# Kernel tuning notes

Measured on AMD Instinct MI355X. Metric: run time of the kernel, lower is better.

The kernel has to match this reference:

```python
import jax, jax.numpy as jnp
import numpy as np

N_CELLS = 50000
HID = 64
DEG = 16
K_NODES = 4  # nodes per cell; cell i owns nodes [4i, 4i+4)
SP = 3


def setup_inputs() -> dict:
    key = jax.random.key(0)
    ks = jax.random.split(key, 12)
    s = 1.0 / np.sqrt(HID)
    inp = {
        'features': jax.random.normal(ks[0], (N_CELLS, HID), jnp.float32),
        'positions': jax.random.normal(ks[1], (K_NODES * N_CELLS, SP), jnp.float32),
        'neighbors': jax.random.randint(ks[2], (N_CELLS, DEG), 0, N_CELLS, jnp.int32),
        # message MLP: Linear(2H+1 -> H), SiLU, Linear(H -> H)
        'W1': jax.random.normal(ks[3], (2 * HID + 1, HID), jnp.float32) * s,
        'b1': jnp.zeros((HID,), jnp.float32),
        'W2': jax.random.normal(ks[4], (HID, HID), jnp.float32) * s,
        'b2': jnp.zeros((HID,), jnp.float32),
        # update MLP: Linear(H + H -> H), SiLU, Linear(H -> H)
        'Wu1': jax.random.normal(ks[5], (2 * HID, HID), jnp.float32) * s,
        'bu1': jnp.zeros((HID,), jnp.float32),
        'Wu2': jax.random.normal(ks[6], (HID, HID), jnp.float32) * s,
        'bu2': jnp.zeros((HID,), jnp.float32),
    }
    return inp


def reference(features, positions, neighbors, W1, b1, W2, b2, Wu1, bu1, Wu2, bu2):
    N, H = features.shape
    # centroid of each cell's owned nodes (cell i -> nodes [K*i, K*i+K))
    cent = positions.reshape(N, K_NODES, SP).mean(axis=1)          # [N, sp]
    fj = features[neighbors]                                       # [N, D, H]
    cj = cent[neighbors]                                           # [N, D, sp]
    # centroid-distance geometric invariant per (cell, neighbor) pair
    geom = jnp.linalg.norm(cent[:, None, :] - cj, axis=-1, keepdims=True)  # [N, D, 1]
    fi = jnp.broadcast_to(features[:, None, :], fj.shape)          # [N, D, H]
    x = jnp.concatenate([fi, fj, geom], axis=-1)                   # [N, D, 2H+1]
    h = jax.nn.silu(x @ W1 + b1) @ W2 + b2                         # [N, D, H]
    msg = h.mean(axis=1)                                           # mean over neighbors
    u = jnp.concatenate([features, msg], axis=-1)                  # [N, 2H]
    upd = jax.nn.silu(u @ Wu1 + bu1) @ Wu2 + bu2
    updated_features = features + upd
    return updated_features, positions
```

## Files before the change

### kernel.cpp

```cpp
#include <hip/hip_runtime.h>


#define DEG 16

typedef __attribute__((ext_vector_type(8))) short short8;
typedef __attribute__((ext_vector_type(4))) float f32x4;
typedef uint2 uint2_a __attribute__((may_alias));
typedef uint4 uint4_a __attribute__((may_alias));

union HbRd { uint4_a u; short8 s; };
union Frag { short8 s; uint4 u; };

__device__ __forceinline__ unsigned f2bf(float f) {
  unsigned u = __float_as_uint(f);
  return (u + 0x7FFFu + ((u >> 16) & 1u)) >> 16;
}
__device__ __forceinline__ float bf2f(unsigned bits16) {
  return __uint_as_float(bits16 << 16);
}
__device__ __forceinline__ float silu(float h) {
  return h / (1.f + __expf(-h));
}
__device__ __forceinline__ float silu_fast(float h) {
  return h * __builtin_amdgcn_rcpf(1.f + __expf(-h));
}

__global__ __launch_bounds__(256) void aux_kernel(
    const float* __restrict__ pos,
    const float* __restrict__ W1, const float* __restrict__ W2,
    const float* __restrict__ Wu1, const float* __restrict__ Wu2,
    float* __restrict__ outpos, float* __restrict__ cent4,
    unsigned short* __restrict__ w1pq, unsigned short* __restrict__ w2t,
    unsigned short* __restrict__ wu1t, unsigned short* __restrict__ wu2b)
{
  int t = blockIdx.x * 256 + threadIdx.x;
  if (t < 150000) {
    ((float4*)outpos)[t] = ((const float4*)pos)[t];
  } else if (t < 174576) {
    const int r = t - 150000;
    if (r < 8192) {
      const int j = r & 7, l = (r >> 3) & 15, q = (r >> 7) & 3;
      const int f = r >> 9, kk = f & 1, mt = f >> 1;
      const int k = kk * 32 + q * 8 + j;
      const int m = mt * 16 + l;
      w1pq[r] = (unsigned short)f2bf(
          (m < 64) ? W1[k * 64 + m] : W1[(k + 64) * 64 + (m - 64)]);
    } else if (r < 12288) {
      const int s = r - 8192;
      const int j = s & 7, l = (s >> 3) & 15, q = (s >> 7) & 3;
      const int f = s >> 9, kk = f & 1, mt = f >> 1;
      const int k = kk * 32 + q * 8 + j;
      w2t[s] = (unsigned short)f2bf(W2[k * 64 + mt * 16 + l]);
    } else if (r < 20480) {
      const int s = r - 12288;
      const int j = s & 7, l = (s >> 3) & 15, q = (s >> 7) & 3;
      const int f = s >> 9, kk = f & 3, mt = f >> 2;
      const int k = kk * 32 + q * 8 + j;
      wu1t[s] = (unsigned short)f2bf(Wu1[k * 64 + mt * 16 + l]);
    } else {
      const int s = r - 20480;
      const int j = s & 7, l = (s >> 3) & 15, q = (s >> 7) & 3;
      const int f = s >> 9, kk = f & 1, nt = f >> 1;
      const int k = kk * 32 + q * 8 + j;
      wu2b[s] = (unsigned short)f2bf(Wu2[k * 64 + nt * 16 + l]);
    }
  } else if (t < 224576) {
    const int i = t - 174576;
    const float4* pp = (const float4*)(pos + 12 * i);
    const float4 a = pp[0], b = pp[1], c = pp[2];
    float4 o;
    o.x = (a.x + a.w + b.z + c.y) * 0.25f;
    o.y = (a.y + b.x + b.w + c.z) * 0.25f;
    o.z = (a.z + b.y + c.x + c.w) * 0.25f;
    o.w = 0.f;
    ((float4*)cent4)[i] = o;
  }
}

__global__ __launch_bounds__(256) void prep_geom_kernel(
    const float* __restrict__ feat,
    const unsigned short* __restrict__ w1pq,
    const float4* __restrict__ cent4,
    const int* __restrict__ nbr,
    unsigned short* __restrict__ featb,
    unsigned short* __restrict__ Pb, unsigned char* __restrict__ Q8,
    float* __restrict__ geomF)
{
  const int b    = blockIdx.x;
  const int lane = threadIdx.x & 63;
  const int wid  = threadIdx.x >> 6;

  if (b >= 782) {
    const int gb  = b - 782;
    const int sub = lane >> 4;
    const int d   = lane & 15;
    const int c   = gb * 16 + wid * 4 + sub;
    const int nj  = nbr[c * DEG + d];
    const float4 ci = cent4[c];
    const float4 cj = cent4[nj];
    const float dx = ci.x - cj.x, dy = ci.y - cj.y, dz = ci.z - cj.z;
    geomF[c * DEG + d] = sqrtf(dx * dx + dy * dy + dz * dz);
    return;
  }

  const int quad = lane >> 4;
  const int l15  = lane & 15;
  const int tile = b * 4 + wid;
  const bool act = (tile < 3125);
  const int  tt  = act ? tile : 3124;
  const int  cr  = tt * 16 + l15;

  short8 xf[2];
  #pragma unroll
  for (int kk = 0; kk < 2; ++kk) {
    const float4 f0 = *(const float4*)(feat + cr * 64 + kk * 32 + quad * 8);
    const float4 f1 = *(const float4*)(feat + cr * 64 + kk * 32 + quad * 8 + 4);
    Frag v;
    v.s[0] = (short)f2bf(f0.x); v.s[1] = (short)f2bf(f0.y);
    v.s[2] = (short)f2bf(f0.z); v.s[3] = (short)f2bf(f0.w);
    v.s[4] = (short)f2bf(f1.x); v.s[5] = (short)f2bf(f1.y);
    v.s[6] = (short)f2bf(f1.z); v.s[7] = (short)f2bf(f1.w);
    xf[kk] = v.s;
    if (act) *(uint4*)(featb + cr * 64 + kk * 32 + quad * 8) = v.u;
  }

  short8 wf[8][2];
  #pragma unroll
  for (int mt = 0; mt < 8; ++mt)
    #pragma unroll
    for (int kk = 0; kk < 2; ++kk)
      wf[mt][kk] = *(const short8*)(w1pq + (((mt * 2 + kk) * 4 + quad) << 7) + l15 * 8);

  f32x4 acc[8] = {};
  #pragma unroll
  for (int kk = 0; kk < 2; ++kk)
    #pragma unroll
    for (int mt = 0; mt < 8; ++mt)
      acc[mt] = __builtin_amdgcn_mfma_f32_16x16x32_bf16(wf[mt][kk], xf[kk], acc[mt], 0, 0, 0);

  if (act) {
    #pragma unroll
    for (int mt = 0; mt < 4; ++mt) {
      uint2 pk;
      pk.x = f2bf(acc[mt][0]) | (f2bf(acc[mt][1]) << 16);
      pk.y = f2bf(acc[mt][2]) | (f2bf(acc[mt][3]) << 16);
      *(uint2*)(Pb + cr * 64 + mt * 16 + quad * 4) = pk;
    }
    #pragma unroll
    for (int mt = 4; mt < 8; ++mt) {
      int w = __builtin_amdgcn_cvt_pk_fp8_f32(acc[mt][0], acc[mt][1], 0, false);
      w = __builtin_amdgcn_cvt_pk_fp8_f32(acc[mt][2], acc[mt][3], w, true);
      *(unsigned int*)(Q8 + cr * 64 + (mt - 4) * 16 + quad * 4) = (unsigned)w;
    }
  }
}

__global__ __launch_bounds__(256) void gather_kernel(
    const unsigned short* __restrict__ Pb,
    const unsigned char* __restrict__ Q8,
    const float* __restrict__ geomF,
    const int* __restrict__ nbr,
    const float* __restrict__ b1, const float* __restrict__ W1,
    unsigned short* __restrict__ sB)
{
  const int lane = threadIdx.x & 63;
  const int wid  = threadIdx.x >> 6;
  const int c    = blockIdx.x * 4 + wid;

  const int   nj = nbr[c * DEG + (lane & 15)];
  const float gv = geomF[c * DEG + (lane & 15)];

  const float pcb = bf2f(Pb[c * 64 + lane]) + b1[lane];
  const float wl  = W1[8192 + lane];

  float acc = 0.f;
  #pragma unroll
  for (int d = 0; d < DEG; ++d) {
    const int   nd = __builtin_amdgcn_readlane(nj, d);
    const float gd = __uint_as_float(
        __builtin_amdgcn_readlane((int)__float_as_uint(gv), d));
    const float qv = __builtin_amdgcn_cvt_f32_fp8((int)Q8[nd * 64 + lane], 0);
    acc += silu_fast(pcb + qv + gd * wl);
  }

  sB[c * 64 + lane] = (unsigned short)f2bf(acc * 0.0625f);
}

__global__ __launch_bounds__(256) void tail_kernel(
    const unsigned short* __restrict__ featb,
    const unsigned short* __restrict__ sB,
    const float* __restrict__ feat,
    const unsigned short* __restrict__ w2t,
    const unsigned short* __restrict__ wu1t,
    const unsigned short* __restrict__ wu2b,
    const float* __restrict__ b2, const float* __restrict__ bu1,
    const float* __restrict__ bu2,
    float* __restrict__ outf)
{
  __shared__ uint4 smem[4 * 288];
  const int lane = threadIdx.x & 63;
  const int wid  = threadIdx.x >> 6;
  const int quad = lane >> 4;
  const int l15  = lane & 15;
  char* Msg = (char*)(smem + wid * 288);
  char* Hb  = Msg + 2304;

  short8 w2f[4][2];
  #pragma unroll
  for (int mt = 0; mt < 4; ++mt)
    #pragma unroll
    for (int kk = 0; kk < 2; ++kk)
      w2f[mt][kk] = *(const short8*)(w2t + (((mt * 2 + kk) * 4 + quad) << 7) + l15 * 8);
  short8 wu1f[4][4];
  #pragma unroll
  for (int mt = 0; mt < 4; ++mt)
    #pragma unroll
    for (int kk = 0; kk < 4; ++kk)
      wu1f[mt][kk] = *(const short8*)(wu1t + (((mt * 4 + kk) * 4 + quad) << 7) + l15 * 8);
  short8 wu2f[4][2];
  #pragma unroll
  for (int nt = 0; nt < 4; ++nt)
    #pragma unroll
    for (int kk = 0; kk < 2; ++kk)
      wu2f[nt][kk] = *(const short8*)(wu2b + (((nt * 2 + kk) * 4 + quad) << 7) + l15 * 8);

  f32x4 b2f[4], bu1f[4];
  #pragma unroll
  for (int mt = 0; mt < 4; ++mt) {
    b2f[mt]  = *(const f32x4*)(b2  + mt * 16 + quad * 4);
    bu1f[mt] = *(const f32x4*)(bu1 + mt * 16 + quad * 4);
  }
  float bu2v[4];
  #pragma unroll
  for (int nt = 0; nt < 4; ++nt) bu2v[nt] = bu2[nt * 16 + l15];

  const int tile = blockIdx.x * 4 + wid;
  const bool act = (tile < 3125);
  const int  tt  = act ? tile : 3124;
  const int  cr  = tt * 16 + l15;

  f32x4 accm[4] = {};
  #pragma unroll
  for (int kk = 0; kk < 2; ++kk) {
    const short8 bf = *(const short8*)(sB + cr * 64 + kk * 32 + quad * 8);
    #pragma unroll
    for (int mt = 0; mt < 4; ++mt)
      accm[mt] = __builtin_amdgcn_mfma_f32_16x16x32_bf16(w2f[mt][kk], bf, accm[mt], 0, 0, 0);
  }
  #pragma unroll
  for (int mt = 0; mt < 4; ++mt) {
    uint2 pk;
    pk.x = f2bf(accm[mt][0] + b2f[mt][0]) | (f2bf(accm[mt][1] + b2f[mt][1]) << 16);
    pk.y = f2bf(accm[mt][2] + b2f[mt][2]) | (f2bf(accm[mt][3] + b2f[mt][3]) << 16);
    *(uint2_a*)(Msg + l15 * 144 + mt * 32 + quad * 8) = pk;
  }
  __threadfence_block();

  f32x4 accu[4] = {};
  #pragma unroll
  for (int kk = 0; kk < 4; ++kk) {
    short8 bf;
    if (kk < 2) {
      bf = *(const short8*)(featb + cr * 64 + kk * 32 + quad * 8);
    } else {
      HbRd t; t.u = *(const uint4_a*)(Msg + l15 * 144 + (kk - 2) * 64 + quad * 16);
      bf = t.s;
    }
    #pragma unroll
    for (int mt = 0; mt < 4; ++mt)
      accu[mt] = __builtin_amdgcn_mfma_f32_16x16x32_bf16(wu1f[mt][kk], bf, accu[mt], 0, 0, 0);
  }
  #pragma unroll
  for (int mt = 0; mt < 4; ++mt) {
    float sv[4];
    #pragma unroll
    for (int rg = 0; rg < 4; ++rg)
      sv[rg] = silu(accu[mt][rg] + bu1f[mt][rg]);
    uint2 pk;
    pk.x = f2bf(sv[0]) | (f2bf(sv[1]) << 16);
    pk.y = f2bf(sv[2]) | (f2bf(sv[3]) << 16);
    *(uint2_a*)(Hb + l15 * 144 + mt * 32 + quad * 8) = pk;
  }
  __threadfence_block();

  f32x4 acc2[4] = {};
  #pragma unroll
  for (int kk = 0; kk < 2; ++kk) {
    HbRd t; t.u = *(const uint4_a*)(Hb + l15 * 144 + kk * 64 + quad * 16);
    const short8 af = t.s;
    #pragma unroll
    for (int nt = 0; nt < 4; ++nt)
      acc2[nt] = __builtin_amdgcn_mfma_f32_16x16x32_bf16(af, wu2f[nt][kk], acc2[nt], 0, 0, 0);
  }
  if (act) {
    #pragma unroll
    for (int nt = 0; nt < 4; ++nt)
      #pragma unroll
      for (int rg = 0; rg < 4; ++rg) {
        const int row = tt * 16 + quad * 4 + rg;
        const int col = nt * 16 + l15;
        outf[row * 64 + col] = feat[row * 64 + col] + acc2[nt][rg] + bu2v[nt];
      }
  }
}

extern "C" void kernel_launch(void* const* d_in, const int* in_sizes, int n_in,
                              void* d_out, int out_size, void* d_ws, size_t ws_size,
                              hipStream_t stream)
{
  const float* feat = (const float*)d_in[0];
  const float* pos  = (const float*)d_in[1];
  const int*   nbr  = (const int*)d_in[2];
  const float* W1   = (const float*)d_in[3];
  const float* b1   = (const float*)d_in[4];
  const float* W2   = (const float*)d_in[5];
  const float* b2   = (const float*)d_in[6];
  const float* Wu1  = (const float*)d_in[7];
  const float* bu1  = (const float*)d_in[8];
  const float* Wu2  = (const float*)d_in[9];
  const float* bu2  = (const float*)d_in[10];
  float* out = (float*)d_out;

  unsigned short* featb = (unsigned short*)d_ws;
  unsigned short* Pb    = (unsigned short*)((char*)d_ws + 6400000);
  unsigned char*  Q8    = (unsigned char*)((char*)d_ws + 12800000);
  float*          geomF = (float*)((char*)d_ws + 16000000);
  unsigned short* sB    = (unsigned short*)((char*)d_ws + 19200000);
  float*          cent4 = (float*)((char*)d_ws + 25600000);
  unsigned short* w1pq  = (unsigned short*)((char*)d_ws + 26400000);
  unsigned short* w2t   = (unsigned short*)((char*)d_ws + 26416384);
  unsigned short* wu1t  = (unsigned short*)((char*)d_ws + 26424576);
  unsigned short* wu2b  = (unsigned short*)((char*)d_ws + 26440960);

  aux_kernel<<<878, 256, 0, stream>>>(pos, W1, W2, Wu1, Wu2, out + 3200000,
                                      cent4, w1pq, w2t, wu1t, wu2b);
  prep_geom_kernel<<<3907, 256, 0, stream>>>(feat, w1pq, (const float4*)cent4,
                                             nbr, featb, Pb, Q8, geomF);
  gather_kernel<<<12500, 256, 0, stream>>>(Pb, Q8, geomF, nbr, b1, W1, sB);
  tail_kernel<<<782, 256, 0, stream>>>(featb, sB, feat, w2t, wu1t, wu2b,
                                       b2, bu1, bu2, out);
}
```

Before: 132.4 us.

## Fuse neighbor gather into tail kernel and split MLP output tiles across waves

Merges the gather kernel and the tail MLP kernel into one kernel. Each block handles a 16-cell tile: the four waves each gather four cells' messages into shared memory, then each wave computes one 16-column slice of every tile GEMM, exchanging intermediates through shared memory with block barriers. This drops the sB round trip through global memory and one launch, and cuts per-wave weight fragment registers. In exchange it adds several __syncthreads and uses fewer, heavier blocks for the gather phase, which may lower latency hiding for the random Q8 loads.

```diff
diff --git a/kernel.cpp b/kernel.cpp
--- a/kernel.cpp
+++ b/kernel.cpp
@@ -155,108 +155,90 @@
   }
 }
 
-__global__ __launch_bounds__(256) void gather_kernel(
+__global__ __launch_bounds__(256) void msg_tail_kernel(
+    const unsigned short* __restrict__ featb,
     const unsigned short* __restrict__ Pb,
     const unsigned char* __restrict__ Q8,
     const float* __restrict__ geomF,
     const int* __restrict__ nbr,
-    const float* __restrict__ b1, const float* __restrict__ W1,
-    unsigned short* __restrict__ sB)
-{
-  const int lane = threadIdx.x & 63;
-  const int wid  = threadIdx.x >> 6;
-  const int c    = blockIdx.x * 4 + wid;
-
-  const int   nj = nbr[c * DEG + (lane & 15)];
-  const float gv = geomF[c * DEG + (lane & 15)];
-
-  const float pcb = bf2f(Pb[c * 64 + lane]) + b1[lane];
-  const float wl  = W1[8192 + lane];
-
-  float acc = 0.f;
-  #pragma unroll
-  for (int d = 0; d < DEG; ++d) {
-    const int   nd = __builtin_amdgcn_readlane(nj, d);
-    const float gd = __uint_as_float(
-        __builtin_amdgcn_readlane((int)__float_as_uint(gv), d));
-    const float qv = __builtin_amdgcn_cvt_f32_fp8((int)Q8[nd * 64 + lane], 0);
-    acc += silu_fast(pcb + qv + gd * wl);
-  }
-
-  sB[c * 64 + lane] = (unsigned short)f2bf(acc * 0.0625f);
-}
-
-__global__ __launch_bounds__(256) void tail_kernel(
-    const unsigned short* __restrict__ featb,
-    const unsigned short* __restrict__ sB,
     const float* __restrict__ feat,
     const unsigned short* __restrict__ w2t,
     const unsigned short* __restrict__ wu1t,
     const unsigned short* __restrict__ wu2b,
+    const float* __restrict__ b1, const float* __restrict__ W1,
     const float* __restrict__ b2, const float* __restrict__ bu1,
     const float* __restrict__ bu2,
     float* __restrict__ outf)
 {
-  __shared__ uint4 smem[4 * 288];
+  __shared__ uint4 smem[432];
+  char* sT  = (char*)smem;
+  char* Msg = sT + 2304;
+  char* Hb  = sT + 4608;
+
   const int lane = threadIdx.x & 63;
   const int wid  = threadIdx.x >> 6;
   const int quad = lane >> 4;
   const int l15  = lane & 15;
-  char* Msg = (char*)(smem + wid * 288);
-  char* Hb  = Msg + 2304;
-
-  short8 w2f[4][2];
-  #pragma unroll
-  for (int mt = 0; mt < 4; ++mt)
-    #pragma unroll
-    for (int kk = 0; kk < 2; ++kk)
-      w2f[mt][kk] = *(const short8*)(w2t + (((mt * 2 + kk) * 4 + quad) << 7) + l15 * 8);
-  short8 wu1f[4][4];
-  #pragma unroll
-  for (int mt = 0; mt < 4; ++mt)
-    #pragma unroll
-    for (int kk = 0; kk < 4; ++kk)
-      wu1f[mt][kk] = *(const short8*)(wu1t + (((mt * 4 + kk) * 4 + quad) << 7) + l15 * 8);
-  short8 wu2f[4][2];
-  #pragma unroll
-  for (int nt = 0; nt < 4; ++nt)
-    #pragma unroll
-    for (int kk = 0; kk < 2; ++kk)
-      wu2f[nt][kk] = *(const short8*)(wu2b + (((nt * 2 + kk) * 4 + quad) << 7) + l15 * 8);
-
-  f32x4 b2f[4], bu1f[4];
-  #pragma unroll
-  for (int mt = 0; mt < 4; ++mt) {
-    b2f[mt]  = *(const f32x4*)(b2  + mt * 16 + quad * 4);
-    bu1f[mt] = *(const f32x4*)(bu1 + mt * 16 + quad * 4);
-  }
-  float bu2v[4];
-  #pragma unroll
-  for (int nt = 0; nt < 4; ++nt) bu2v[nt] = bu2[nt * 16 + l15];
-
-  const int tile = blockIdx.x * 4 + wid;
-  const bool act = (tile < 3125);
-  const int  tt  = act ? tile : 3124;
-  const int  cr  = tt * 16 + l15;
-
-  f32x4 accm[4] = {};
+  const int tile = blockIdx.x;
+
+  const float b1l = b1[lane];
+  const float wl  = W1[8192 + lane];
+
+  #pragma unroll
+  for (int i = 0; i < 4; ++i) {
+    const int c  = tile * 16 + wid * 4 + i;
+    const int cs = __builtin_amdgcn_readfirstlane(c);
+    const int*   nrow = nbr   + cs * DEG;
+    const float* grow = geomF + cs * DEG;
+
+    const float pcb = bf2f(Pb[cs * 64 + lane]) + b1l;
+
+    float acc = 0.f;
+    #pragma unroll
+    for (int d = 0; d < DEG; ++d) {
+      const int   nd = nrow[d];
+      const float gd = grow[d];
+      const float qv = __builtin_amdgcn_cvt_f32_fp8((int)Q8[nd * 64 + lane], 0);
+      acc += silu_fast(pcb + qv + gd * wl);
+    }
+    ((unsigned short*)(sT + (wid * 4 + i) * 144))[lane] =
+        (unsigned short)f2bf(acc * 0.0625f);
+  }
+
+  short8 w2f[2], wu1f[4], wu2f[2];
+  #pragma unroll
+  for (int kk = 0; kk < 2; ++kk)
+    w2f[kk]  = *(const short8*)(w2t  + (((wid * 2 + kk) * 4 + quad) << 7) + l15 * 8);
+  #pragma unroll
+  for (int kk = 0; kk < 4; ++kk)
+    wu1f[kk] = *(const short8*)(wu1t + (((wid * 4 + kk) * 4 + quad) << 7) + l15 * 8);
+  #pragma unroll
+  for (int kk = 0; kk < 2; ++kk)
+    wu2f[kk] = *(const short8*)(wu2b + (((wid * 2 + kk) * 4 + quad) << 7) + l15 * 8);
+
+  const f32x4 b2f  = *(const f32x4*)(b2  + wid * 16 + quad * 4);
+  const f32x4 bu1f = *(const f32x4*)(bu1 + wid * 16 + quad * 4);
+  const float bu2v = bu2[wid * 16 + l15];
+
+  __syncthreads();
+
+  f32x4 accm = {};
   #pragma unroll
   for (int kk = 0; kk < 2; ++kk) {
-    const short8 bf = *(const short8*)(sB + cr * 64 + kk * 32 + quad * 8);
-    #pragma unroll
-    for (int mt = 0; mt < 4; ++mt)
-      accm[mt] = __builtin_amdgcn_mfma_f32_16x16x32_bf16(w2f[mt][kk], bf, accm[mt], 0, 0, 0);
-  }
-  #pragma unroll
-  for (int mt = 0; mt < 4; ++mt) {
+    HbRd t; t.u = *(const uint4_a*)(sT + l15 * 144 + kk * 64 + quad * 16);
+    accm = __builtin_amdgcn_mfma_f32_16x16x32_bf16(w2f[kk], t.s, accm, 0, 0, 0);
+  }
+  __syncthreads();
+  {
     uint2 pk;
-    pk.x = f2bf(accm[mt][0] + b2f[mt][0]) | (f2bf(accm[mt][1] + b2f[mt][1]) << 16);
-    pk.y = f2bf(accm[mt][2] + b2f[mt][2]) | (f2bf(accm[mt][3] + b2f[mt][3]) << 16);
-    *(uint2_a*)(Msg + l15 * 144 + mt * 32 + quad * 8) = pk;
-  }
-  __threadfence_block();
-
-  f32x4 accu[4] = {};
+    pk.x = f2bf(accm[0] + b2f[0]) | (f2bf(accm[1] + b2f[1]) << 16);
+    pk.y = f2bf(accm[2] + b2f[2]) | (f2bf(accm[3] + b2f[3]) << 16);
+    *(uint2_a*)(Msg + l15 * 144 + wid * 32 + quad * 8) = pk;
+  }
+  __syncthreads();
+
+  const int cr = tile * 16 + l15;
+  f32x4 accu = {};
   #pragma unroll
   for (int kk = 0; kk < 4; ++kk) {
     short8 bf;
@@ -266,41 +248,31 @@
       HbRd t; t.u = *(const uint4_a*)(Msg + l15 * 144 + (kk - 2) * 64 + quad * 16);
       bf = t.s;
     }
-    #pragma unroll
-    for (int mt = 0; mt < 4; ++mt)
-      accu[mt] = __builtin_amdgcn_mfma_f32_16x16x32_bf16(wu1f[mt][kk], bf, accu[mt], 0, 0, 0);
-  }
-  #pragma unroll
-  for (int mt = 0; mt < 4; ++mt) {
+    accu = __builtin_amdgcn_mfma_f32_16x16x32_bf16(wu1f[kk], bf, accu, 0, 0, 0);
+  }
+  {
     float sv[4];
     #pragma unroll
     for (int rg = 0; rg < 4; ++rg)
-      sv[rg] = silu(accu[mt][rg] + bu1f[mt][rg]);
+      sv[rg] = silu(accu[rg] + bu1f[rg]);
     uint2 pk;
     pk.x = f2bf(sv[0]) | (f2bf(sv[1]) << 16);
     pk.y = f2bf(sv[2]) | (f2bf(sv[3]) << 16);
-    *(uint2_a*)(Hb + l15 * 144 + mt * 32 + quad * 8) = pk;
-  }
-  __threadfence_block();
-
-  f32x4 acc2[4] = {};
+    *(uint2_a*)(Hb + l15 * 144 + wid * 32 + quad * 8) = pk;
+  }
+  __syncthreads();
+
+  f32x4 acc2 = {};
   #pragma unroll
   for (int kk = 0; kk < 2; ++kk) {
     HbRd t; t.u = *(const uint4_a*)(Hb + l15 * 144 + kk * 64 + quad * 16);
-    const short8 af = t.s;
-    #pragma unroll
-    for (int nt = 0; nt < 4; ++nt)
-      acc2[nt] = __builtin_amdgcn_mfma_f32_16x16x32_bf16(af, wu2f[nt][kk], acc2[nt], 0, 0, 0);
-  }
-  if (act) {
-    #pragma unroll
-    for (int nt = 0; nt < 4; ++nt)
-      #pragma unroll
-      for (int rg = 0; rg < 4; ++rg) {
-        const int row = tt * 16 + quad * 4 + rg;
-        const int col = nt * 16 + l15;
-        outf[row * 64 + col] = feat[row * 64 + col] + acc2[nt][rg] + bu2v[nt];
-      }
+    acc2 = __builtin_amdgcn_mfma_f32_16x16x32_bf16(t.s, wu2f[kk], acc2, 0, 0, 0);
+  }
+  #pragma unroll
+  for (int rg = 0; rg < 4; ++rg) {
+    const int row = tile * 16 + quad * 4 + rg;
+    const int col = wid * 16 + l15;
+    outf[row * 64 + col] = feat[row * 64 + col] + acc2[rg] + bu2v;
   }
 }
 
@@ -325,7 +297,6 @@
   unsigned short* Pb    = (unsigned short*)((char*)d_ws + 6400000);
   unsigned char*  Q8    = (unsigned char*)((char*)d_ws + 12800000);
   float*          geomF = (float*)((char*)d_ws + 16000000);
-  unsigned short* sB    = (unsigned short*)((char*)d_ws + 19200000);
   float*          cent4 = (float*)((char*)d_ws + 25600000);
   unsigned short* w1pq  = (unsigned short*)((char*)d_ws + 26400000);
   unsigned short* w2t   = (unsigned short*)((char*)d_ws + 26416384);
@@ -336,7 +307,7 @@
                                       cent4, w1pq, w2t, wu1t, wu2b);
   prep_geom_kernel<<<3907, 256, 0, stream>>>(feat, w1pq, (const float4*)cent4,
                                              nbr, featb, Pb, Q8, geomF);
-  gather_kernel<<<12500, 256, 0, stream>>>(Pb, Q8, geomF, nbr, b1, W1, sB);
-  tail_kernel<<<782, 256, 0, stream>>>(featb, sB, feat, w2t, wu1t, wu2b,
-                                       b2, bu1, bu2, out);
-}
+  msg_tail_kernel<<<3125, 256, 0, stream>>>(featb, Pb, Q8, geomF, nbr, feat,
+                                            w2t, wu1t, wu2b,
+                                            b1, W1, b2, bu1, bu2, out);
+}
```

After: 121.8 us. 1.09x faster.
